# Performance work log

Measured on AMD Instinct MI355X. Metric: run time of the kernel, lower is better.

The kernel has to match this reference:

```python
import jax, jax.numpy as jnp
from jax import lax
import numpy as np

B, C_IN, H, W = 4, 3, 128, 128
K, D = 8192, 16  # num_embeddings, embedding_size (= encoder out channels)


def _conv(x, w, b):
    # x: (B,C,H,W), w: (O,I,3,3) OIHW, VALID padding, stride 1
    y = lax.conv_general_dilated(x, w, (1, 1), 'VALID',
                                 dimension_numbers=('NCHW', 'OIHW', 'NCHW'))
    return y + b[None, :, None, None]


def _conv_t(x, w, b):
    # transpose conv, stride 1, k=3: correlate with flipped/transposed kernel, pad 2
    # w: (I,O,3,3) -> flip spatial, swap to OIHW
    wk = jnp.flip(w, (2, 3)).transpose(1, 0, 2, 3)
    y = lax.conv_general_dilated(x, wk, (1, 1), [(2, 2), (2, 2)],
                                 dimension_numbers=('NCHW', 'OIHW', 'NCHW'))
    return y + b[None, :, None, None]


def setup_inputs() -> dict:
    key = jax.random.key(0)
    ks = jax.random.split(key, 14)
    g = lambda k, shp, fan: jax.random.normal(k, shp, jnp.float32) / np.float32(np.sqrt(fan))
    return {
        'x':   jax.random.normal(ks[0], (B, C_IN, H, W), jnp.float32),
        'ew1': g(ks[1], (4, C_IN, 3, 3), C_IN * 9), 'eb1': jnp.zeros((4,), jnp.float32),
        'ew2': g(ks[2], (8, 4, 3, 3), 4 * 9),       'eb2': jnp.zeros((8,), jnp.float32),
        'ew3': g(ks[3], (16, 8, 3, 3), 8 * 9),      'eb3': jnp.zeros((16,), jnp.float32),
        'dw1': g(ks[4], (16, 8, 3, 3), 16 * 9),     'db1': jnp.zeros((8,), jnp.float32),
        'dw2': g(ks[5], (8, 4, 3, 3), 8 * 9),       'db2': jnp.zeros((4,), jnp.float32),
        'dw3': g(ks[6], (4, C_IN, 3, 3), 4 * 9),    'db3': jnp.zeros((C_IN,), jnp.float32),
        'codebook': jax.random.normal(ks[7], (K, D), jnp.float32) * 0.02,
    }


def reference(x, ew1, eb1, ew2, eb2, ew3, eb3, dw1, db1, dw2, db2, dw3, db3, codebook):
    # encode
    z = jax.nn.selu(_conv(x, ew1, eb1))
    z = jax.nn.selu(_conv(z, ew2, eb2))
    z = _conv(z, ew3, eb3)                      # (B, D, h, w)
    b, d, h, w = z.shape
    zf = z.transpose(0, 2, 3, 1).reshape(-1, d)  # (N, D) flattened latents
    # ||z - e||^2 = ||z||^2 - 2 z.e + ||e||^2, argmin over codebook rows
    d2 = ((zf * zf).sum(1, keepdims=True)
          - 2.0 * (zf @ codebook.T)
          + (codebook * codebook).sum(1)[None, :])  # (N, K)
    idx = jnp.argmin(d2, axis=1)                 # (N,) int32
    zq = codebook[idx].reshape(b, h, w, d).transpose(0, 3, 1, 2)  # gather + reshape
    # decode
    y = jax.nn.selu(_conv_t(zq, dw1, db1))
    y = jax.nn.selu(_conv_t(y, dw2, db2))
    y = _conv_t(y, dw3, db3)                     # (B, C_IN, H, W)
    return (y, idx)
```

## Files before the change

kernel.cpp:

```cpp
#include <hip/hip_runtime.h>
#include <math.h>

#define BATCH 4
#define DLAT 16
#define KCB 8192
#define HLAT 122
#define PIX (HLAT*HLAT)
#define NLAT (BATCH*PIX)
#define NT32 (KCB/32)
#define ROWSB 32
#define NVQBLK 1861
#define NWAVE 8
#define TW (NT32/NWAVE)
#define CAPW 1024
#define NCONVBLK 3721

typedef _Float16 half8 __attribute__((ext_vector_type(8)));
typedef float f32x16 __attribute__((ext_vector_type(16)));

__device__ __forceinline__ float selu_np(float x) {
    const float scale = 1.0507009873554805f, alpha = 1.6732632423543772f;
    if (x > 0.f) return __fmul_rn(scale, x);
    return __fmul_rn(scale, __fmul_rn(alpha, expm1f(x)));
}

template<int CI, int CO, int HIN, int WIN, bool DOSELU>
__global__ void conv3x3_np(const float* __restrict__ in, const float* __restrict__ w,
                           const float* __restrict__ bias, float* __restrict__ out) {
    constexpr int HO = HIN - 2, WO = WIN - 2;
    int tid = blockIdx.x * blockDim.x + threadIdx.x;
    constexpr int total = BATCH * CO * HO * WO;
    if (tid >= total) return;
    int j = tid % WO; int t = tid / WO;
    int i = t % HO;   t /= HO;
    int o = t % CO;   int b = t / CO;
    float acc = 0.f;
    for (int c = 0; c < CI; ++c) {
        const float* ip = in + ((b * CI + c) * HIN + i) * WIN + j;
        const float* wp = w + ((o * CI + c) * 3) * 3;
        #pragma unroll
        for (int p = 0; p < 3; ++p)
            #pragma unroll
            for (int q = 0; q < 3; ++q)
                acc = __fmaf_rn(ip[p * WIN + q], wp[p * 3 + q], acc);
    }
    acc = __fadd_rn(acc, bias[o]);
    out[tid] = DOSELU ? selu_np(acc) : acc;
}

__global__ void conv3_last_np(const float* __restrict__ in, const float* __restrict__ w,
                              const float* __restrict__ bias, float* __restrict__ zf,
                              _Float16* __restrict__ zh, float* __restrict__ blockmax) {
    constexpr int CI = 8, HIN = 124, WIN = 124, WO = 122;
    __shared__ float sred[4];
    int tid = blockIdx.x * 256 + threadIdx.x;
    int o  = tid & 15;
    int pp = tid >> 4;
    int b = pp / PIX, pix = pp % PIX;
    int i = pix / WO, j = pix % WO;
    float acc = 0.f;
    for (int c = 0; c < CI; ++c) {
        const float* ip = in + ((b * CI + c) * HIN + i) * WIN + j;
        const float* wp = w + ((o * CI + c) * 3) * 3;
        #pragma unroll
        for (int p = 0; p < 3; ++p)
            #pragma unroll
            for (int q = 0; q < 3; ++q)
                acc = __fmaf_rn(ip[p * WIN + q], wp[p * 3 + q], acc);
    }
    acc = __fadd_rn(acc, bias[o]);
    zf[tid] = acc;
    zh[tid] = (_Float16)acc;
    float m = fabsf(acc);
    #pragma unroll
    for (int off = 32; off; off >>= 1) m = fmaxf(m, __shfl_xor(m, off));
    if ((threadIdx.x & 63) == 0) sred[threadIdx.x >> 6] = m;
    __syncthreads();
    if (threadIdx.x == 0)
        blockmax[blockIdx.x] = fmaxf(fmaxf(sred[0], sred[1]), fmaxf(sred[2], sred[3]));
}

__global__ void reduce_zmax(const float* __restrict__ bm, unsigned* __restrict__ scal) {
    __shared__ float sred[4];
    float m = 0.f;
    for (int i = threadIdx.x; i < NCONVBLK; i += 256) m = fmaxf(m, bm[i]);
    #pragma unroll
    for (int off = 32; off; off >>= 1) m = fmaxf(m, __shfl_xor(m, off));
    if ((threadIdx.x & 63) == 0) sred[threadIdx.x >> 6] = m;
    __syncthreads();
    if (threadIdx.x == 0)
        scal[0] = __float_as_uint(fmaxf(fmaxf(sred[0], sred[1]), fmaxf(sred[2], sred[3])));
}

__device__ __forceinline__ float pairwise16_sq(const float* v) {
    float a[16];
    #pragma unroll
    for (int d = 0; d < 16; ++d) a[d] = __fmul_rn(v[d], v[d]);
    float r0 = __fadd_rn(a[0], a[8]),  r1 = __fadd_rn(a[1], a[9]);
    float r2 = __fadd_rn(a[2], a[10]), r3 = __fadd_rn(a[3], a[11]);
    float r4 = __fadd_rn(a[4], a[12]), r5 = __fadd_rn(a[5], a[13]);
    float r6 = __fadd_rn(a[6], a[14]), r7 = __fadd_rn(a[7], a[15]);
    return __fadd_rn(__fadd_rn(__fadd_rn(r0, r1), __fadd_rn(r2, r3)),
                     __fadd_rn(__fadd_rn(r4, r5), __fadd_rn(r6, r7)));
}

__device__ __forceinline__ void load16(const float* __restrict__ p, float* v) {
    const float4* r = (const float4*)p;
    float4 v0 = r[0], v1 = r[1], v2 = r[2], v3 = r[3];
    v[0]=v0.x; v[1]=v0.y; v[2]=v0.z; v[3]=v0.w;
    v[4]=v1.x; v[5]=v1.y; v[6]=v1.z; v[7]=v1.w;
    v[8]=v2.x; v[9]=v2.y; v[10]=v2.z; v[11]=v2.w;
    v[12]=v3.x; v[13]=v3.y; v[14]=v3.z; v[15]=v3.w;
}

__device__ __forceinline__ float np_d2(const float* zr, float A, const float* e16, float cnk) {
    float g = 0.f;
    #pragma unroll
    for (int d = 0; d < 16; ++d) g = __fmaf_rn(zr[d], e16[d], g);
    return __fadd_rn(__fmaf_rn(-2.f, g, A), cnk);
}

__global__ void init_scal(unsigned* scal) { scal[0] = 0u; scal[1] = 0u; }

__global__ void cbprep(const float* __restrict__ cb, float* __restrict__ cn,
                       _Float16* __restrict__ cbB, unsigned* __restrict__ scal) {
    int k = blockIdx.x * 256 + threadIdx.x;
    float v[16];
    load16(cb + (size_t)k * DLAT, v);
    float C = pairwise16_sq(v);
    cn[k] = C;
    float m = C;
    #pragma unroll
    for (int off = 32; off; off >>= 1) m = fmaxf(m, __shfl_xor(m, off));
    if ((threadIdx.x & 63) == 0) atomicMax(&scal[1], __float_as_uint(m));
    int tile = k >> 5, col = k & 31;
    #pragma unroll
    for (int d = 0; d < 16; ++d) {
        int ln = (d >> 3) * 32 + col;
        cbB[(size_t)tile * 512 + ln * 8 + (d & 7)] = (_Float16)v[d];
    }
}

#define DROW(reg, lanehi) (((reg) & 3) + 8 * ((reg) >> 2) + 4 * (lanehi))

__global__ __launch_bounds__(512, 4) void vq_mfma(
        const _Float16* __restrict__ zh, const float* __restrict__ zf,
        const _Float16* __restrict__ cbB, const float* __restrict__ cn,
        const float* __restrict__ cb, const unsigned* __restrict__ scal,
        float* __restrict__ idx_out, float* __restrict__ zq) {
    __shared__ unsigned list[CAPW];
    __shared__ float resd[CAPW];
    __shared__ float smin[NWAVE][ROWSB];
    __shared__ unsigned lcnt;
    const int tid = threadIdx.x;
    const int w = tid >> 6, lane = tid & 63;
    const int lanehi = lane >> 5;
    const int R0 = blockIdx.x * ROWSB;
    const f32x16 zero16 = {0.f,0.f,0.f,0.f,0.f,0.f,0.f,0.f,0.f,0.f,0.f,0.f,0.f,0.f,0.f,0.f};
    if (tid == 0) lcnt = 0;

    int ar = R0 + (lane & 31);
    if (ar >= NLAT) ar = NLAT - 1;
    half8 a = *(const half8*)(zh + (size_t)ar * DLAT + lanehi * 8);

    float zmaxf = __uint_as_float(scal[0]);
    float en    = sqrtf(__uint_as_float(scal[1]));
    float errG  = 4.f * zmaxf * en * 9.765625e-4f * 1.03f
                + 6.104e-5f * (16.f * zmaxf + 4.f * en);
    float slack = (16.f * zmaxf * zmaxf + 8.f * zmaxf * en + en * en) * 1.2e-7f;
    float DELTA = 4.f * errG + 2.f * slack + 1e-6f;

    const int t0 = w * TW, t1 = t0 + TW;

    float m[16];
    #pragma unroll
    for (int r = 0; r < 16; ++r) m[r] = INFINITY;

    #pragma unroll 2
    for (int t = t0; t < t1; ++t) {
        half8 b = *(const half8*)(cbB + (size_t)t * 512 + lane * 8);
        float cnv = cn[t * 32 + (lane & 31)];
        f32x16 D = __builtin_amdgcn_mfma_f32_32x32x16_f16(a, b, zero16, 0, 0, 0);
        #pragma unroll
        for (int r = 0; r < 16; ++r)
            m[r] = fminf(m[r], __fmaf_rn(-2.f, D[r], cnv));
    }
    #pragma unroll
    for (int r = 0; r < 16; ++r) {
        float v = m[r];
        v = fminf(v, __shfl_xor(v, 1));
        v = fminf(v, __shfl_xor(v, 2));
        v = fminf(v, __shfl_xor(v, 4));
        v = fminf(v, __shfl_xor(v, 8));
        v = fminf(v, __shfl_xor(v, 16));
        m[r] = v;
    }
    if ((lane & 31) == 0) {
        #pragma unroll
        for (int r = 0; r < 16; ++r)
            smin[w][DROW(r, lanehi)] = m[r];
    }
    __syncthreads();
    #pragma unroll
    for (int r = 0; r < 16; ++r) {
        int row = DROW(r, lanehi);
        float v = INFINITY;
        #pragma unroll
        for (int ww = 0; ww < NWAVE; ++ww) v = fminf(v, smin[ww][row]);
        m[r] = v + DELTA;
    }

    #pragma unroll 2
    for (int t = t0; t < t1; ++t) {
        half8 b = *(const half8*)(cbB + (size_t)t * 512 + lane * 8);
        float cnv = cn[t * 32 + (lane & 31)];
        f32x16 D = __builtin_amdgcn_mfma_f32_32x32x16_f16(a, b, zero16, 0, 0, 0);
        bool anyp = false;
        #pragma unroll
        for (int r = 0; r < 16; ++r)
            anyp |= (__fmaf_rn(-2.f, D[r], cnv) <= m[r]);
        if (__ballot(anyp)) {
            #pragma unroll
            for (int r = 0; r < 16; ++r) {
                bool pred = (__fmaf_rn(-2.f, D[r], cnv) <= m[r]);
                unsigned long long bal = __ballot(pred);
                if (bal) {
                    unsigned nb = (unsigned)__popcll(bal);
                    unsigned base = 0;
                    if (lane == 0) base = atomicAdd(&lcnt, nb);
                    base = __shfl(base, 0);
                    unsigned pos = base + (unsigned)__popcll(bal & ((1ull << lane) - 1ull));
                    if (pred && pos < CAPW) {
                        unsigned rs = (unsigned)DROW(r, lanehi);
                        list[pos] = (rs << 13) | (unsigned)(t * 32 + (lane & 31));
                    }
                }
            }
        }
    }
    __syncthreads();
    unsigned cnt = lcnt;

    if (cnt <= CAPW) {
        for (unsigned i = tid; i < cnt; i += 512) {
            unsigned e = list[i];
            int n = R0 + (int)(e >> 13);
            if (n >= NLAT) n = NLAT - 1;
            int k = (int)(e & 8191);
            float zr[16], e16[16];
            load16(zf + (size_t)n * DLAT, zr);
            float A = pairwise16_sq(zr);
            load16(cb + (size_t)k * DLAT, e16);
            resd[i] = np_d2(zr, A, e16, cn[k]);
        }
    }
    __syncthreads();

    if (tid < ROWSB) {
        int r = R0 + tid;
        if (r < NLAT) {
            float bd = INFINITY; int bk = 0x7fffffff;
            if (cnt <= CAPW) {
                for (unsigned i = 0; i < cnt; ++i) {
                    unsigned e = list[i];
                    if ((int)(e >> 13) == tid) {
                        float d2 = resd[i]; int k = (int)(e & 8191);
                        if (d2 < bd || (d2 == bd && k < bk)) { bd = d2; bk = k; }
                    }
                }
            } else {
                float zr[16];
                load16(zf + (size_t)r * DLAT, zr);
                float A = pairwise16_sq(zr);
                for (int k = 0; k < KCB; ++k) {
                    float e16[16];
                    load16(cb + (size_t)k * DLAT, e16);
                    float d2 = np_d2(zr, A, e16, cn[k]);
                    if (d2 < bd) { bd = d2; bk = k; }
                }
            }
            idx_out[r] = (float)bk;
            int b = r / PIX, pix = r % PIX;
            const float* e = cb + (size_t)bk * DLAT;
            #pragma unroll
            for (int d = 0; d < DLAT; ++d) zq[((size_t)(b * DLAT + d)) * PIX + pix] = e[d];
        }
    }
}

template<int CI, int CO, int HIN, int WIN, bool DOSELU>
__global__ void convt3x3(const float* __restrict__ in, const float* __restrict__ w,
                         const float* __restrict__ bias, float* __restrict__ out) {
    constexpr int HO = HIN + 2, WO = WIN + 2;
    int tid = blockIdx.x * blockDim.x + threadIdx.x;
    constexpr int total = BATCH * CO * HO * WO;
    if (tid >= total) return;
    int j = tid % WO; int t = tid / WO;
    int i = t % HO;   t /= HO;
    int o = t % CO;   int b = t / CO;
    float acc = bias[o];
    for (int c = 0; c < CI; ++c) {
        const float* ip = in + ((b * CI + c) * HIN) * WIN;
        const float* wp = w + ((c * CO + o) * 3) * 3;
        #pragma unroll
        for (int p = 0; p < 3; ++p) {
            int ii = i + p - 2;
            if (ii < 0 || ii >= HIN) continue;
            #pragma unroll
            for (int q = 0; q < 3; ++q) {
                int jj = j + q - 2;
                if (jj < 0 || jj >= WIN) continue;
                acc += ip[ii * WIN + jj] * wp[(2 - p) * 3 + (2 - q)];
            }
        }
    }
    const float scale = 1.0507009873554805f, alpha = 1.6732632423543772f;
    out[tid] = DOSELU ? (acc > 0.f ? scale * acc : scale * alpha * (expf(acc) - 1.f)) : acc;
}

extern "C" void kernel_launch(void* const* d_in, const int* in_sizes, int n_in,
                              void* d_out, int out_size, void* d_ws, size_t ws_size,
                              hipStream_t stream) {
    const float* x   = (const float*)d_in[0];
    const float* ew1 = (const float*)d_in[1];  const float* eb1 = (const float*)d_in[2];
    const float* ew2 = (const float*)d_in[3];  const float* eb2 = (const float*)d_in[4];
    const float* ew3 = (const float*)d_in[5];  const float* eb3 = (const float*)d_in[6];
    const float* dw1 = (const float*)d_in[7];  const float* db1 = (const float*)d_in[8];
    const float* dw2 = (const float*)d_in[9];  const float* db2 = (const float*)d_in[10];
    const float* dw3 = (const float*)d_in[11]; const float* db3 = (const float*)d_in[12];
    const float* cb  = (const float*)d_in[13];

    float* out_y   = (float*)d_out;
    float* out_idx = (float*)d_out + 196608;

    float*     ws   = (float*)d_ws;
    float*     zf   = ws;
    float*     e1   = ws + 952576;
    float*     e2   = ws + 1206592;
    float*     fZq  = ws + 952576;
    float*     fB   = ws + 1905152;
    float*     fA   = ws + 2397184;
    _Float16*  zh   = (_Float16*)(ws + 2651200);
    _Float16*  cbB  = (_Float16*)(ws + 3127488);
    float*     cn   = ws + 3193024;
    unsigned*  scal = (unsigned*)(ws + 3201216);
    float*     bmax = ws + 3201218;

    const int TPB = 256;

    init_scal<<<1, 1, 0, stream>>>(scal);

    conv3x3_np<3, 4, 128, 128, true ><<<993,  TPB, 0, stream>>>(x,  ew1, eb1, e1);
    conv3x3_np<4, 8, 126, 126, true ><<<1922, TPB, 0, stream>>>(e1, ew2, eb2, e2);
    conv3_last_np<<<NCONVBLK, TPB, 0, stream>>>(e2, ew3, eb3, zf, zh, bmax);
    reduce_zmax<<<1, TPB, 0, stream>>>(bmax, scal);

    cbprep<<<32, TPB, 0, stream>>>(cb, cn, cbB, scal);
    vq_mfma<<<NVQBLK, 512, 0, stream>>>(zh, zf, cbB, cn, cb, scal, out_idx, fZq);

    convt3x3<16, 8, 122, 122, true ><<<1922, TPB, 0, stream>>>(fZq, dw1, db1, fB);
    convt3x3<8, 4, 124, 124, true ><<<993,  TPB, 0, stream>>>(fB,  dw2, db2, fA);
    convt3x3<4, 3, 126, 126, false><<<768,  TPB, 0, stream>>>(fA,  dw3, db3, out_y);
}
```

Baseline: 233.2 us.

## Process 64 latent rows per VQ block with two MFMA fragments sharing codebook loads

The VQ search kernel now handles 64 latent rows per block instead of 32. Each wave holds two A fragments and runs two MFMAs per codebook tile, so each loaded codebook tile and norm value serves twice as many rows. This halves the block count and per-row codebook traffic, at the cost of doubled running-min registers and a lower occupancy hint of 2 blocks per CU. The shared candidate list keeps its capacity of 1024 while serving twice as many rows, so the overflow fallback may trigger more often.

```diff
diff --git a/kernel.cpp b/kernel.cpp
--- a/kernel.cpp
+++ b/kernel.cpp
@@ -8,8 +8,8 @@
 #define PIX (HLAT*HLAT)
 #define NLAT (BATCH*PIX)
 #define NT32 (KCB/32)
-#define ROWSB 32
-#define NVQBLK 1861
+#define ROWSB 64
+#define NVQBLK 931
 #define NWAVE 8
 #define TW (NT32/NWAVE)
 #define CAPW 1024
@@ -143,7 +143,7 @@
 
 #define DROW(reg, lanehi) (((reg) & 3) + 8 * ((reg) >> 2) + 4 * (lanehi))
 
-__global__ __launch_bounds__(512, 4) void vq_mfma(
+__global__ __launch_bounds__(512, 2) void vq_mfma(
         const _Float16* __restrict__ zh, const float* __restrict__ zf,
         const _Float16* __restrict__ cbB, const float* __restrict__ cn,
         const float* __restrict__ cb, const unsigned* __restrict__ scal,
@@ -159,9 +159,13 @@
     const f32x16 zero16 = {0.f,0.f,0.f,0.f,0.f,0.f,0.f,0.f,0.f,0.f,0.f,0.f,0.f,0.f,0.f,0.f};
     if (tid == 0) lcnt = 0;
 
-    int ar = R0 + (lane & 31);
-    if (ar >= NLAT) ar = NLAT - 1;
-    half8 a = *(const half8*)(zh + (size_t)ar * DLAT + lanehi * 8);
+    half8 a[2];
+    #pragma unroll
+    for (int f = 0; f < 2; ++f) {
+        int ar = R0 + f * 32 + (lane & 31);
+        if (ar >= NLAT) ar = NLAT - 1;
+        a[f] = *(const half8*)(zh + (size_t)ar * DLAT + lanehi * 8);
+    }
 
     float zmaxf = __uint_as_float(scal[0]);
     float en    = sqrtf(__uint_as_float(scal[1]));
@@ -172,67 +176,81 @@
 
     const int t0 = w * TW, t1 = t0 + TW;
 
-    float m[16];
-    #pragma unroll
-    for (int r = 0; r < 16; ++r) m[r] = INFINITY;
+    float m[2][16];
+    #pragma unroll
+    for (int f = 0; f < 2; ++f)
+        #pragma unroll
+        for (int r = 0; r < 16; ++r) m[f][r] = INFINITY;
 
     #pragma unroll 2
     for (int t = t0; t < t1; ++t) {
         half8 b = *(const half8*)(cbB + (size_t)t * 512 + lane * 8);
         float cnv = cn[t * 32 + (lane & 31)];
-        f32x16 D = __builtin_amdgcn_mfma_f32_32x32x16_f16(a, b, zero16, 0, 0, 0);
-        #pragma unroll
-        for (int r = 0; r < 16; ++r)
-            m[r] = fminf(m[r], __fmaf_rn(-2.f, D[r], cnv));
-    }
-    #pragma unroll
-    for (int r = 0; r < 16; ++r) {
-        float v = m[r];
-        v = fminf(v, __shfl_xor(v, 1));
-        v = fminf(v, __shfl_xor(v, 2));
-        v = fminf(v, __shfl_xor(v, 4));
-        v = fminf(v, __shfl_xor(v, 8));
-        v = fminf(v, __shfl_xor(v, 16));
-        m[r] = v;
-    }
+        #pragma unroll
+        for (int f = 0; f < 2; ++f) {
+            f32x16 D = __builtin_amdgcn_mfma_f32_32x32x16_f16(a[f], b, zero16, 0, 0, 0);
+            #pragma unroll
+            for (int r = 0; r < 16; ++r)
+                m[f][r] = fminf(m[f][r], __fmaf_rn(-2.f, D[r], cnv));
+        }
+    }
+    #pragma unroll
+    for (int f = 0; f < 2; ++f)
+        #pragma unroll
+        for (int r = 0; r < 16; ++r) {
+            float v = m[f][r];
+            v = fminf(v, __shfl_xor(v, 1));
+            v = fminf(v, __shfl_xor(v, 2));
+            v = fminf(v, __shfl_xor(v, 4));
+            v = fminf(v, __shfl_xor(v, 8));
+            v = fminf(v, __shfl_xor(v, 16));
+            m[f][r] = v;
+        }
     if ((lane & 31) == 0) {
         #pragma unroll
-        for (int r = 0; r < 16; ++r)
-            smin[w][DROW(r, lanehi)] = m[r];
-    }
-    __syncthreads();
-    #pragma unroll
-    for (int r = 0; r < 16; ++r) {
-        int row = DROW(r, lanehi);
-        float v = INFINITY;
-        #pragma unroll
-        for (int ww = 0; ww < NWAVE; ++ww) v = fminf(v, smin[ww][row]);
-        m[r] = v + DELTA;
-    }
+        for (int f = 0; f < 2; ++f)
+            #pragma unroll
+            for (int r = 0; r < 16; ++r)
+                smin[w][f * 32 + DROW(r, lanehi)] = m[f][r];
+    }
+    __syncthreads();
+    #pragma unroll
+    for (int f = 0; f < 2; ++f)
+        #pragma unroll
+        for (int r = 0; r < 16; ++r) {
+            int row = f * 32 + DROW(r, lanehi);
+            float v = INFINITY;
+            #pragma unroll
+            for (int ww = 0; ww < NWAVE; ++ww) v = fminf(v, smin[ww][row]);
+            m[f][r] = v + DELTA;
+        }
 
     #pragma unroll 2
     for (int t = t0; t < t1; ++t) {
         half8 b = *(const half8*)(cbB + (size_t)t * 512 + lane * 8);
         float cnv = cn[t * 32 + (lane & 31)];
-        f32x16 D = __builtin_amdgcn_mfma_f32_32x32x16_f16(a, b, zero16, 0, 0, 0);
-        bool anyp = false;
-        #pragma unroll
-        for (int r = 0; r < 16; ++r)
-            anyp |= (__fmaf_rn(-2.f, D[r], cnv) <= m[r]);
-        if (__ballot(anyp)) {
-            #pragma unroll
-            for (int r = 0; r < 16; ++r) {
-                bool pred = (__fmaf_rn(-2.f, D[r], cnv) <= m[r]);
-                unsigned long long bal = __ballot(pred);
-                if (bal) {
-                    unsigned nb = (unsigned)__popcll(bal);
-                    unsigned base = 0;
-                    if (lane == 0) base = atomicAdd(&lcnt, nb);
-                    base = __shfl(base, 0);
-                    unsigned pos = base + (unsigned)__popcll(bal & ((1ull << lane) - 1ull));
-                    if (pred && pos < CAPW) {
-                        unsigned rs = (unsigned)DROW(r, lanehi);
-                        list[pos] = (rs << 13) | (unsigned)(t * 32 + (lane & 31));
+        #pragma unroll
+        for (int f = 0; f < 2; ++f) {
+            f32x16 D = __builtin_amdgcn_mfma_f32_32x32x16_f16(a[f], b, zero16, 0, 0, 0);
+            bool anyp = false;
+            #pragma unroll
+            for (int r = 0; r < 16; ++r)
+                anyp |= (__fmaf_rn(-2.f, D[r], cnv) <= m[f][r]);
+            if (__ballot(anyp)) {
+                #pragma unroll
+                for (int r = 0; r < 16; ++r) {
+                    bool pred = (__fmaf_rn(-2.f, D[r], cnv) <= m[f][r]);
+                    unsigned long long bal = __ballot(pred);
+                    if (bal) {
+                        unsigned nb = (unsigned)__popcll(bal);
+                        unsigned base = 0;
+                        if (lane == 0) base = atomicAdd(&lcnt, nb);
+                        base = __shfl(base, 0);
+                        unsigned pos = base + (unsigned)__popcll(bal & ((1ull << lane) - 1ull));
+                        if (pred && pos < CAPW) {
+                            unsigned rs = (unsigned)(f * 32 + DROW(r, lanehi));
+                            list[pos] = (rs << 13) | (unsigned)(t * 32 + (lane & 31));
+                        }
                     }
                 }
             }
```

Result: slower. 251.2 us (+7.7%).
